# Optimization experiments

Measured on AMD Instinct MI355X. Metric: run time of the kernel, lower is better.

The kernel has to match this reference:

```python
import jax, jax.numpy as jnp
import numpy as np
from jax import lax

WINDOW_SIZE = 11
SIGMA = 1.5
CHANNELS = 3
C1 = 0.01 ** 2
C2 = 0.03 ** 2


def _create_window():
    coords = jnp.arange(WINDOW_SIZE, dtype=jnp.float32) - WINDOW_SIZE // 2
    g = jnp.exp(-coords ** 2 / (2.0 * SIGMA ** 2))
    g = g / g.sum()
    w2d = g[:, None] * g[None, :]                      # (11, 11)
    # depthwise kernel, OIHW with groups=channels -> (C, 1, k, k)
    return jnp.broadcast_to(w2d, (CHANNELS, 1, WINDOW_SIZE, WINDOW_SIZE))


def _dwconv(x, window):
    pad = WINDOW_SIZE // 2
    return lax.conv_general_dilated(
        x, window,
        window_strides=(1, 1),
        padding=[(pad, pad), (pad, pad)],
        dimension_numbers=('NCHW', 'OIHW', 'NCHW'),
        feature_group_count=CHANNELS,
    )


def setup_inputs() -> dict:
    key = jax.random.key(0)
    k1, k2 = jax.random.split(key)
    pred = jax.random.uniform(k1, (32, 3, 512, 512), dtype=jnp.float32)
    target = jax.random.uniform(k2, (32, 3, 512, 512), dtype=jnp.float32)
    return {"pred": pred, "target": target}


def reference(pred, target):
    pred = pred.astype(jnp.float32)
    target = target.astype(jnp.float32)
    window = _create_window()

    mu1 = _dwconv(pred, window)
    mu2 = _dwconv(target, window)
    mu1_sq = mu1 * mu1
    mu2_sq = mu2 * mu2
    mu1_mu2 = mu1 * mu2
    sigma1_sq = _dwconv(pred * pred, window) - mu1_sq
    sigma2_sq = _dwconv(target * target, window) - mu2_sq
    sigma12 = _dwconv(pred * target, window) - mu1_mu2

    ssim_map = ((2.0 * mu1_mu2 + C1) * (2.0 * sigma12 + C2)) / (
        (mu1_sq + mu2_sq + C1) * (sigma1_sq + sigma2_sq + C2))
    return 1.0 - ssim_map.mean()
```

## Files before the change

kernel.cpp:

```cpp
#include <hip/hip_runtime.h>
#include <hip/hip_bf16.h>
#include <math.h>

#define BLOCK 256
#define IMG 512
#define SW 84
#define RSTR 40
#define NBLOCKS 3072
#define NACC 128
#define N_TOTAL 25165824.0f

typedef float f32x4 __attribute__((ext_vector_type(4)));
typedef short s16x8 __attribute__((ext_vector_type(8)));

struct WB { unsigned short b[11]; float corr; };
union FR { unsigned int u[4]; s16x8 s; };

__device__ __forceinline__ unsigned int pk2(float a, float b) {
    union { __hip_bfloat162 h; unsigned int u; } cv;
    cv.h = __float22bfloat162_rn(make_float2(a, b));
    return cv.u;
}

__device__ __forceinline__ void stage5(unsigned short (*sq)[16][SW],
                                       int r, int i, float4 xv, float4 yv) {
    *(uint2*)&sq[0][r][4*i] = make_uint2(pk2(xv.x,xv.y), pk2(xv.z,xv.w));
    *(uint2*)&sq[1][r][4*i] = make_uint2(pk2(yv.x,yv.y), pk2(yv.z,yv.w));
    *(uint2*)&sq[2][r][4*i] = make_uint2(pk2(xv.x*xv.x,xv.y*xv.y), pk2(xv.z*xv.z,xv.w*xv.w));
    *(uint2*)&sq[3][r][4*i] = make_uint2(pk2(yv.x*yv.x,yv.y*yv.y), pk2(yv.z*yv.z,yv.w*yv.w));
    *(uint2*)&sq[4][r][4*i] = make_uint2(pk2(xv.x*yv.x,xv.y*yv.y), pk2(xv.z*yv.z,xv.w*yv.w));
}

__global__ __launch_bounds__(BLOCK, 3)
void ssim_tiled(const float* __restrict__ pred,
                const float* __restrict__ targ,
                float* __restrict__ accum, WB wb) {
    __shared__ unsigned short s_w[3][16][32];
    __shared__ unsigned short s_q[5][16][SW];
    __shared__ unsigned short s_ring[5][64][RSTR];

    const int tid = threadIdx.x;
    for (int e = tid; e < 3 * 512; e += BLOCK) {
        const int mat = e >> 9;
        const int m   = (e >> 5) & 15;
        const int k   = e & 31;
        int idx;
        if (mat == 0) idx = k - m - 3;
        else          idx = (k - m - (mat == 2 ? 16 : 0)) & 31;
        s_w[mat][m][k] = (idx >= 0 && idx <= 10) ? wb.b[idx] : (unsigned short)0;
    }

    const int bx    = blockIdx.x;
    const int plane = bx >> 5;
    const int rem   = bx & 31;
    const int tx    = rem >> 2;
    const int ry    = rem & 3;
    const int C0    = tx * 64;
    const int R0    = ry * 128;

    const float* P = pred + (size_t)plane * (IMG * IMG);
    const float* T = targ + (size_t)plane * (IMG * IMG);

    const int w    = tid >> 6;
    const int lane = tid & 63;
    const int l15  = lane & 15;
    const int quad = lane >> 4;

    const int slotA = w * 80 + lane;
    const int rA = slotA / 20, iA = slotA % 20;
    const int colA = C0 - 8 + 4 * iA;
    const bool okcA = (colA >= 0) && (colA + 4 <= IMG);
    const bool hasB = (lane < 16);
    const int slotB = w * 80 + 64 + l15;
    const int rB = slotB / 20, iB = slotB % 20;
    const int colB = C0 - 8 + 4 * iB;
    const bool okcB = (colB >= 0) && (colB + 4 <= IMG);

    const float corr = wb.corr;
    const float C1v = 0.0001f, C2v = 0.0009f;
    const f32x4 z = {0.f, 0.f, 0.f, 0.f};
    float lsum = 0.f;

    float4 xA, yA, xB, yB;
    {
        const int gr = R0 - 5 + rA;
        if (okcA && gr >= 0) {
            xA = *(const float4*)(P + ((size_t)gr << 9) + colA);
            yA = *(const float4*)(T + ((size_t)gr << 9) + colA);
        } else { xA = make_float4(0,0,0,0); yA = make_float4(0,0,0,0); }
        const int grB = R0 - 5 + rB;
        if (hasB && okcB && grB >= 0) {
            xB = *(const float4*)(P + ((size_t)grB << 9) + colB);
            yB = *(const float4*)(T + ((size_t)grB << 9) + colB);
        } else { xB = make_float4(0,0,0,0); yB = make_float4(0,0,0,0); }
    }
    __syncthreads();

    FR bw;  bw.s  = *(const s16x8*)&s_w[0][l15][quad * 8];
    FR aw0; aw0.s = *(const s16x8*)&s_w[1][l15][quad * 8];
    FR aw1; aw1.s = *(const s16x8*)&s_w[2][l15][quad * 8];

    stage5(s_q, rA, iA, xA, yA);
    if (hasB) stage5(s_q, rB, iB, xB, yB);
    __syncthreads();

    const int rcol = 16 * w + l15;

    for (int s = 0; s < 9; ++s) {
        float4 nxA, nyA, nxB, nyB;
        if (s < 8) {
            const int gr = R0 - 5 + 16 * (s + 1) + rA;
            if (okcA && gr < IMG) {
                nxA = *(const float4*)(P + ((size_t)gr << 9) + colA);
                nyA = *(const float4*)(T + ((size_t)gr << 9) + colA);
            } else { nxA = make_float4(0,0,0,0); nyA = make_float4(0,0,0,0); }
            const int grB = R0 - 5 + 16 * (s + 1) + rB;
            if (hasB && okcB && grB < IMG) {
                nxB = *(const float4*)(P + ((size_t)grB << 9) + colB);
                nyB = *(const float4*)(T + ((size_t)grB << 9) + colB);
            } else { nxB = make_float4(0,0,0,0); nyB = make_float4(0,0,0,0); }
        }

        {
            FR a0, a1, a2, a3, a4;
            a0.s = *(const s16x8*)&s_q[0][l15][16*w + 8*quad];
            a1.s = *(const s16x8*)&s_q[1][l15][16*w + 8*quad];
            a2.s = *(const s16x8*)&s_q[2][l15][16*w + 8*quad];
            a3.s = *(const s16x8*)&s_q[3][l15][16*w + 8*quad];
            a4.s = *(const s16x8*)&s_q[4][l15][16*w + 8*quad];
            f32x4 d0 = __builtin_amdgcn_mfma_f32_16x16x32_bf16(a0.s, bw.s, z, 0, 0, 0);
            f32x4 d1 = __builtin_amdgcn_mfma_f32_16x16x32_bf16(a1.s, bw.s, z, 0, 0, 0);
            f32x4 d2 = __builtin_amdgcn_mfma_f32_16x16x32_bf16(a2.s, bw.s, z, 0, 0, 0);
            f32x4 d3 = __builtin_amdgcn_mfma_f32_16x16x32_bf16(a3.s, bw.s, z, 0, 0, 0);
            f32x4 d4 = __builtin_amdgcn_mfma_f32_16x16x32_bf16(a4.s, bw.s, z, 0, 0, 0);
            const int pb = (16 * s + 4 * quad) & 31;
            *(uint2*)&s_ring[0][rcol][pb] = make_uint2(pk2(d0[0],d0[1]), pk2(d0[2],d0[3]));
            *(uint2*)&s_ring[1][rcol][pb] = make_uint2(pk2(d1[0],d1[1]), pk2(d1[2],d1[3]));
            *(uint2*)&s_ring[2][rcol][pb] = make_uint2(pk2(d2[0],d2[1]), pk2(d2[2],d2[3]));
            *(uint2*)&s_ring[3][rcol][pb] = make_uint2(pk2(d3[0],d3[1]), pk2(d3[2],d3[3]));
            *(uint2*)&s_ring[4][rcol][pb] = make_uint2(pk2(d4[0],d4[1]), pk2(d4[2],d4[3]));
        }

        if (s >= 1) {
            const int t = s - 1;
            const FR aw = (t & 1) ? aw1 : aw0;
            f32x4 acc[5];
#pragma unroll
            for (int q = 0; q < 5; ++q) {
                FR b; b.s = *(const s16x8*)&s_ring[q][rcol][quad * 8];
                acc[q] = __builtin_amdgcn_mfma_f32_16x16x32_bf16(aw.s, b.s, z, 0, 0, 0);
            }
#pragma unroll
            for (int i = 0; i < 4; ++i) {
                const float mu1 = acc[0][i] * corr;
                const float mu2 = acc[1][i] * corr;
                const float exx = acc[2][i] * corr;
                const float eyy = acc[3][i] * corr;
                const float exy = acc[4][i] * corr;
                const float mu1s = mu1 * mu1;
                const float mu2s = mu2 * mu2;
                const float mu12 = mu1 * mu2;
                const float sg1  = exx - mu1s;
                const float sg2  = eyy - mu2s;
                const float sg12 = exy - mu12;
                const float num  = fmaf(2.f, mu12, C1v) * fmaf(2.f, sg12, C2v);
                const float den  = (mu1s + mu2s + C1v) * (sg1 + sg2 + C2v);
                lsum = fmaf(num, __builtin_amdgcn_rcpf(den), lsum);
            }
        }

        __syncthreads();

        if (s < 8) {
            stage5(s_q, rA, iA, nxA, nyA);
            if (hasB) stage5(s_q, rB, iB, nxB, nyB);
            __syncthreads();
        }
    }

#pragma unroll
    for (int off = 32; off > 0; off >>= 1) lsum += __shfl_down(lsum, off, 64);
    if (lane == 0) atomicAdd(&accum[(bx * 4 + w) & (NACC - 1)], lsum);
}

__global__ void ssim_finalize(const float* __restrict__ accum, float* __restrict__ out) {
    const int l = threadIdx.x;
    float v = accum[l] + accum[l + 64];
#pragma unroll
    for (int off = 32; off > 0; off >>= 1) v += __shfl_down(v, off, 64);
    if (l == 0) out[0] = 1.0f - v * (1.0f / N_TOTAL);
}

extern "C" void kernel_launch(void* const* d_in, const int* in_sizes, int n_in,
                              void* d_out, int out_size, void* d_ws, size_t ws_size,
                              hipStream_t stream) {
    const float* pred = (const float*)d_in[0];
    const float* targ = (const float*)d_in[1];
    float* out = (float*)d_out;
    float* ws  = (float*)d_ws;

    WB wb;
    {
        double gg[11], sum = 0.0;
        for (int k = 0; k < 11; ++k) {
            const double d = (double)(k - 5);
            gg[k] = exp(-d * d / 4.5);
            sum += gg[k];
        }
        double sbf = 0.0;
        for (int k = 0; k < 11; ++k) {
            union { float f; unsigned int u; } cv;
            cv.f = (float)(gg[k] / sum);
            const unsigned int r = (cv.u + 0x7fffu + ((cv.u >> 16) & 1u)) >> 16;
            wb.b[k] = (unsigned short)r;
            union { float f; unsigned int u; } bk;
            bk.u = r << 16;
            sbf += (double)bk.f;
        }
        wb.corr = (float)(1.0 / (sbf * sbf));
    }

    hipMemsetAsync(ws, 0, NACC * sizeof(float), stream);
    ssim_tiled<<<NBLOCKS, BLOCK, 0, stream>>>(pred, targ, ws, wb);
    ssim_finalize<<<1, 64, 0, stream>>>(ws, out);
}
```

Baseline: 265.4 us.

## Prefetch two row-steps ahead, fold window normalization into constants, pad LDS stride

Global loads are now issued two stages ahead using a double-buffered register set, and the stage loop is fully unrolled. The aim is to hide more global-memory latency behind the MFMA work. The per-element correction multiplies are removed by rescaling the SSIM constants on the host, so only the second-moment terms need one multiply each. The staging tile stride grows from 84 to 88, likely to change LDS bank mapping. The extra prefetch buffers raise register pressure, which may hurt occupancy under launch_bounds(256,3).

Result: faster. 257.6 us (-3.0%).

```diff
diff --git a/kernel.cpp b/kernel.cpp
--- a/kernel.cpp
+++ b/kernel.cpp
@@ -4,7 +4,7 @@
 
 #define BLOCK 256
 #define IMG 512
-#define SW 84
+#define SW 88
 #define RSTR 40
 #define NBLOCKS 3072
 #define NACC 128
@@ -13,7 +13,7 @@
 typedef float f32x4 __attribute__((ext_vector_type(4)));
 typedef short s16x8 __attribute__((ext_vector_type(8)));
 
-struct WB { unsigned short b[11]; float corr; };
+struct WB { unsigned short b[11]; float c2; float k1; float k2; };
 union FR { unsigned int u[4]; s16x8 s; };
 
 __device__ __forceinline__ unsigned int pk2(float a, float b) {
@@ -29,6 +29,24 @@
     *(uint2*)&sq[2][r][4*i] = make_uint2(pk2(xv.x*xv.x,xv.y*xv.y), pk2(xv.z*xv.z,xv.w*xv.w));
     *(uint2*)&sq[3][r][4*i] = make_uint2(pk2(yv.x*yv.x,yv.y*yv.y), pk2(yv.z*yv.z,yv.w*yv.w));
     *(uint2*)&sq[4][r][4*i] = make_uint2(pk2(xv.x*yv.x,xv.y*yv.y), pk2(xv.z*yv.z,xv.w*yv.w));
+}
+
+__device__ __forceinline__ void load_set(const float* __restrict__ P,
+                                         const float* __restrict__ T,
+                                         int R0, int step,
+                                         int rA, int colA, bool okcA,
+                                         bool hasB, int rB, int colB, bool okcB,
+                                         float4& xA, float4& yA, float4& xB, float4& yB) {
+    const int gr = R0 - 5 + 16 * step + rA;
+    if (okcA && gr >= 0 && gr < IMG) {
+        xA = *(const float4*)(P + ((size_t)gr << 9) + colA);
+        yA = *(const float4*)(T + ((size_t)gr << 9) + colA);
+    } else { xA = make_float4(0,0,0,0); yA = make_float4(0,0,0,0); }
+    const int grB = R0 - 5 + 16 * step + rB;
+    if (hasB && okcB && grB >= 0 && grB < IMG) {
+        xB = *(const float4*)(P + ((size_t)grB << 9) + colB);
+        yB = *(const float4*)(T + ((size_t)grB << 9) + colB);
+    } else { xB = make_float4(0,0,0,0); yB = make_float4(0,0,0,0); }
 }
 
 __global__ __launch_bounds__(BLOCK, 3)
@@ -76,49 +94,32 @@
     const int colB = C0 - 8 + 4 * iB;
     const bool okcB = (colB >= 0) && (colB + 4 <= IMG);
 
-    const float corr = wb.corr;
-    const float C1v = 0.0001f, C2v = 0.0009f;
+    const float c2 = wb.c2, K1 = wb.k1, K2 = wb.k2;
     const f32x4 z = {0.f, 0.f, 0.f, 0.f};
     float lsum = 0.f;
 
-    float4 xA, yA, xB, yB;
-    {
-        const int gr = R0 - 5 + rA;
-        if (okcA && gr >= 0) {
-            xA = *(const float4*)(P + ((size_t)gr << 9) + colA);
-            yA = *(const float4*)(T + ((size_t)gr << 9) + colA);
-        } else { xA = make_float4(0,0,0,0); yA = make_float4(0,0,0,0); }
-        const int grB = R0 - 5 + rB;
-        if (hasB && okcB && grB >= 0) {
-            xB = *(const float4*)(P + ((size_t)grB << 9) + colB);
-            yB = *(const float4*)(T + ((size_t)grB << 9) + colB);
-        } else { xB = make_float4(0,0,0,0); yB = make_float4(0,0,0,0); }
-    }
+    float4 pxA, pyA, pxB, pyB;
+    load_set(P, T, R0, 0, rA, colA, okcA, hasB, rB, colB, okcB, pxA, pyA, pxB, pyB);
+    float4 sxA[2], syA[2], sxB[2], syB[2];
+    load_set(P, T, R0, 1, rA, colA, okcA, hasB, rB, colB, okcB,
+             sxA[1], syA[1], sxB[1], syB[1]);
     __syncthreads();
 
     FR bw;  bw.s  = *(const s16x8*)&s_w[0][l15][quad * 8];
     FR aw0; aw0.s = *(const s16x8*)&s_w[1][l15][quad * 8];
     FR aw1; aw1.s = *(const s16x8*)&s_w[2][l15][quad * 8];
 
-    stage5(s_q, rA, iA, xA, yA);
-    if (hasB) stage5(s_q, rB, iB, xB, yB);
+    stage5(s_q, rA, iA, pxA, pyA);
+    if (hasB) stage5(s_q, rB, iB, pxB, pyB);
     __syncthreads();
 
     const int rcol = 16 * w + l15;
 
+#pragma unroll
     for (int s = 0; s < 9; ++s) {
-        float4 nxA, nyA, nxB, nyB;
-        if (s < 8) {
-            const int gr = R0 - 5 + 16 * (s + 1) + rA;
-            if (okcA && gr < IMG) {
-                nxA = *(const float4*)(P + ((size_t)gr << 9) + colA);
-                nyA = *(const float4*)(T + ((size_t)gr << 9) + colA);
-            } else { nxA = make_float4(0,0,0,0); nyA = make_float4(0,0,0,0); }
-            const int grB = R0 - 5 + 16 * (s + 1) + rB;
-            if (hasB && okcB && grB < IMG) {
-                nxB = *(const float4*)(P + ((size_t)grB << 9) + colB);
-                nyB = *(const float4*)(T + ((size_t)grB << 9) + colB);
-            } else { nxB = make_float4(0,0,0,0); nyB = make_float4(0,0,0,0); }
+        if (s < 7) {
+            load_set(P, T, R0, s + 2, rA, colA, okcA, hasB, rB, colB, okcB,
+                     sxA[s & 1], syA[s & 1], sxB[s & 1], syB[s & 1]);
         }
 
         {
@@ -142,8 +143,7 @@
         }
 
         if (s >= 1) {
-            const int t = s - 1;
-            const FR aw = (t & 1) ? aw1 : aw0;
+            const FR aw = ((s - 1) & 1) ? aw1 : aw0;
             f32x4 acc[5];
 #pragma unroll
             for (int q = 0; q < 5; ++q) {
@@ -152,28 +152,27 @@
             }
 #pragma unroll
             for (int i = 0; i < 4; ++i) {
-                const float mu1 = acc[0][i] * corr;
-                const float mu2 = acc[1][i] * corr;
-                const float exx = acc[2][i] * corr;
-                const float eyy = acc[3][i] * corr;
-                const float exy = acc[4][i] * corr;
-                const float mu1s = mu1 * mu1;
-                const float mu2s = mu2 * mu2;
-                const float mu12 = mu1 * mu2;
-                const float sg1  = exx - mu1s;
-                const float sg2  = eyy - mu2s;
-                const float sg12 = exy - mu12;
-                const float num  = fmaf(2.f, mu12, C1v) * fmaf(2.f, sg12, C2v);
-                const float den  = (mu1s + mu2s + C1v) * (sg1 + sg2 + C2v);
-                lsum = fmaf(num, __builtin_amdgcn_rcpf(den), lsum);
+                const float u1  = acc[0][i];
+                const float u2  = acc[1][i];
+                const float m11 = u1 * u1;
+                const float m22 = u2 * u2;
+                const float m12 = u1 * u2;
+                const float e11 = acc[2][i] * c2;
+                const float e22 = acc[3][i] * c2;
+                const float e12 = acc[4][i] * c2;
+                const float A = fmaf(2.f, m12, K1);
+                const float B = fmaf(2.f, e12 - m12, K2);
+                const float C = m11 + m22 + K1;
+                const float D = (e11 + e22) - (m11 + m22) + K2;
+                lsum = fmaf(A * B, __builtin_amdgcn_rcpf(C * D), lsum);
             }
         }
 
         __syncthreads();
 
         if (s < 8) {
-            stage5(s_q, rA, iA, nxA, nyA);
-            if (hasB) stage5(s_q, rB, iB, nxB, nyB);
+            stage5(s_q, rA, iA, sxA[(s + 1) & 1], syA[(s + 1) & 1]);
+            if (hasB) stage5(s_q, rB, iB, sxB[(s + 1) & 1], syB[(s + 1) & 1]);
             __syncthreads();
         }
     }
@@ -217,7 +216,10 @@
             bk.u = r << 16;
             sbf += (double)bk.f;
         }
-        wb.corr = (float)(1.0 / (sbf * sbf));
+        const double s2 = sbf * sbf;
+        wb.c2 = (float)s2;
+        wb.k1 = (float)(0.0001 * s2 * s2);
+        wb.k2 = (float)(0.0009 * s2 * s2);
     }
 
     hipMemsetAsync(ws, 0, NACC * sizeof(float), stream);
```
